# Kernel tuning notes

Hardware: AMD Instinct MI355X
Metric: run time of the kernel (lower is better)

## Reference

```python
import jax, jax.numpy as jnp
import numpy as np

N_BOXES = 1_000_000
EPS = 1e-6


def box2corners(box):
    """(..., 5) [x,y,w,h,angle] -> (..., 4, 2) corners (mmcv box2corners)."""
    x, y, w, h, a = (box[..., i] for i in range(5))
    dx = jnp.asarray([0.5, -0.5, -0.5, 0.5], box.dtype) * w[..., None]  # (...,4)
    dy = jnp.asarray([0.5, 0.5, -0.5, -0.5], box.dtype) * h[..., None]
    cos, sin = jnp.cos(a)[..., None], jnp.sin(a)[..., None]
    cx = dx * cos - dy * sin + x[..., None]
    cy = dx * sin + dy * cos + y[..., None]
    return jnp.stack([cx, cy], axis=-1)


def box_intersection(c1, c2):
    """All 4x4 edge-pair segment intersections. c1,c2: (N,4,2).
    Returns pts (N,4,4,2), mask (N,4,4)."""
    roll = jnp.array([1, 2, 3, 0])
    line1 = jnp.concatenate([c1, c1[:, roll, :]], axis=-1)  # (N,4,4): x1,y1,x2,y2
    line2 = jnp.concatenate([c2, c2[:, roll, :]], axis=-1)
    l1 = line1[:, :, None, :]  # (N,4,1,4)
    l2 = line2[:, None, :, :]  # (N,1,4,4)
    x1, y1, x2, y2 = l1[..., 0], l1[..., 1], l1[..., 2], l1[..., 3]
    x3, y3, x4, y4 = l2[..., 0], l2[..., 1], l2[..., 2], l2[..., 3]
    num = (y4 - y3) * (x2 - x1) - (x4 - x3) * (y2 - y1)
    den_t = (x4 - x3) * (y1 - y3) - (y4 - y3) * (x1 - x3)
    safe = jnp.where(num == 0.0, 1.0, num)
    t = jnp.where(num == 0.0, -1.0, den_t / safe)
    mask_t = (t > 0) & (t < 1)
    den_u = (x2 - x1) * (y1 - y3) - (y2 - y1) * (x1 - x3)
    u = jnp.where(num == 0.0, -1.0, -den_u / safe)
    mask_u = (u > 0) & (u < 1)
    mask = mask_t & mask_u
    t2 = den_t / (num + 1e-8)
    pts = jnp.stack([x1 + t2 * (x2 - x1), y1 + t2 * (y2 - y1)], axis=-1)
    pts = pts * mask[..., None].astype(pts.dtype)
    return pts, mask


def box1_in_box2(c1, c2):
    """Which corners of c1 lie inside box c2. (N,4,2)x(N,4,2)->(N,4) bool."""
    a = c2[:, 0:1, :]
    b = c2[:, 1:2, :]
    d = c2[:, 3:4, :]
    ab, ad, am = b - a, d - a, c1 - a
    pab = jnp.sum(ab * am, -1) / jnp.sum(ab * ab, -1)
    pad_ = jnp.sum(ad * am, -1) / jnp.sum(ad * ad, -1)
    e = 1e-6
    return (pab > -e) & (pab < 1 + e) & (pad_ > -e) & (pad_ < 1 + e)


def intersection_area(c1, c2):
    """Differentiable rotated-box intersection area via convex polygon clipping."""
    inter_pts, inter_mask = box_intersection(c1, c2)
    m1 = box1_in_box2(c1, c2)
    m2 = box1_in_box2(c2, c1)
    n = c1.shape[0]
    verts = jnp.concatenate([c1, c2, inter_pts.reshape(n, 16, 2)], axis=1)  # (N,24,2)
    mask = jnp.concatenate([m1, m2, inter_mask.reshape(n, 16)], axis=1)     # (N,24)
    k = jnp.sum(mask, axis=-1)  # num valid vertices per box
    mf = mask.astype(verts.dtype)
    mean = jnp.sum(verts * mf[..., None], axis=1, keepdims=True) / \
        jnp.maximum(k, 1).astype(verts.dtype)[:, None, None]
    vn = verts - mean
    # sort valid vertices counterclockwise by angle around centroid; invalid last
    ang = jnp.where(mask, jnp.arctan2(vn[..., 1], vn[..., 0]), 1e9)
    order = jnp.argsort(ang, axis=-1)
    vs = jnp.take_along_axis(verts, order[..., None], axis=1)  # (N,24,2)
    idx = jnp.arange(24)
    nxt = jnp.where(idx[None, :] + 1 < k[:, None], idx[None, :] + 1, 0)
    v_next = jnp.take_along_axis(vs, nxt[..., None], axis=1)
    cross = vs[..., 0] * v_next[..., 1] - vs[..., 1] * v_next[..., 0]
    valid = idx[None, :] < k[:, None]
    return jnp.abs(jnp.sum(jnp.where(valid, cross, 0.0), axis=-1)) * 0.5


def fpdiou_loss(pred, target):
    c1 = box2corners(pred)
    c2 = box2corners(target)
    inter = intersection_area(c1, c2)
    area1 = pred[:, 2] * pred[:, 3]
    area2 = target[:, 2] * target[:, 3]
    iou = inter / (area1 + area2 - inter)
    iou = jnp.maximum(iou, EPS)
    # corner-distance term (detached in original via .detach().cpu().numpy())
    p = jax.lax.stop_gradient(c1)
    g = jax.lax.stop_gradient(c2)
    ps = jnp.take_along_axis(p, jnp.argsort(p[..., 0], axis=-1)[..., None], axis=1)
    gs = jnp.take_along_axis(g, jnp.argsort(g[..., 0], axis=-1)[..., None], axis=1)
    d = 2.0 * (gs[:, 0, 0] - ps[:, 0, 0]) ** 2 \
        + (ps[:, 1, 0] - gs[:, 1, 0]) ** 2 + (ps[:, 1, 1] - gs[:, 1, 1]) ** 2 \
        + (ps[:, 2, 0] - gs[:, 2, 0]) ** 2 + (ps[:, 2, 1] - gs[:, 2, 1]) ** 2 \
        + (ps[:, 3, 0] - gs[:, 3, 0]) ** 2 + (ps[:, 3, 1] - gs[:, 3, 1]) ** 2
    res = d / (4.0 * 1024.0 ** 2)
    loss = 1.0 - iou + res  # mode='linear'
    return jnp.mean(loss)   # reduction='mean', loss_weight=1.0


def setup_inputs() -> dict:
    key = jax.random.key(0)
    k1, k2, k3, k4 = jax.random.split(key, 4)
    xy = jax.random.uniform(k1, (N_BOXES, 2), minval=0.0, maxval=1024.0)
    wh = jax.random.uniform(k2, (N_BOXES, 2), minval=8.0, maxval=96.0)
    ang = jax.random.uniform(k3, (N_BOXES, 1), minval=-np.pi / 2, maxval=np.pi / 2)
    pred = jnp.concatenate([xy, wh, ang], axis=-1).astype(jnp.float32)
    scale = jnp.asarray([4.0, 4.0, 3.0, 3.0, 0.1], jnp.float32)
    target = pred + jax.random.normal(k4, (N_BOXES, 5), jnp.float32) * scale
    target = target.at[:, 2:4].set(jnp.maximum(target[:, 2:4], 4.0))
    return {"pred": pred, "target": target}


def reference(pred, target):
    return fpdiou_loss(pred, target)
```

## Files before the change

kernel.cpp:

```cpp
#include <hip/hip_runtime.h>

#define BS 64
#define NVMAX 16

__device__ __forceinline__ void sort4_by_x(const float* x, const float* y,
                                           float* sx, float* sy) {
    int rk[4];
#pragma unroll
    for (int a = 0; a < 4; a++) {
        int r = 0;
#pragma unroll
        for (int b = 0; b < 4; b++) {
            r += (x[b] < x[a]) || (x[b] == x[a] && b < a);
        }
        rk[a] = r;
    }
#pragma unroll
    for (int r = 0; r < 4; r++) {
        float vx = 0.f, vy = 0.f;
#pragma unroll
        for (int a = 0; a < 4; a++) {
            if (rk[a] == r) { vx = x[a]; vy = y[a]; }
        }
        sx[r] = vx; sy[r] = vy;
    }
}

__device__ __forceinline__ float pseudo_angle(float dx, float dy) {
    float s = fabsf(dx) + fabsf(dy);
    float r = (s == 0.f) ? 0.f : (1.f - dx / s);
    return copysignf(r, dy);
}

__global__ __launch_bounds__(BS, 2)
void fpdiou_kernel(const float* __restrict__ pred, const float* __restrict__ tgt,
                   float* __restrict__ partial, int n)
{
    __shared__ float s_vx[NVMAX * BS];
    __shared__ float s_vy[NVMAX * BS];
    __shared__ float s_p [NVMAX * BS];

    const int tid = threadIdx.x;
    const int i = blockIdx.x * BS + tid;
    float loss = 0.f;

    if (i < n) {
        const float* pp = pred + (size_t)i * 5;
        const float* gg = tgt  + (size_t)i * 5;
        const float pw = pp[2], ph = pp[3];
        const float gw = gg[2], gh = gg[3];

        float c1x[4], c1y[4], c2x[4], c2y[4];
        {
            const float DX[4] = {0.5f, -0.5f, -0.5f, 0.5f};
            const float DY[4] = {0.5f,  0.5f, -0.5f, -0.5f};
            float s, c;
            sincosf(pp[4], &s, &c);
            float x = pp[0], y = pp[1];
#pragma unroll
            for (int q = 0; q < 4; q++) {
                float dx = DX[q] * pw, dy = DY[q] * ph;
                c1x[q] = dx * c - dy * s + x;
                c1y[q] = dx * s + dy * c + y;
            }
            sincosf(gg[4], &s, &c);
            x = gg[0]; y = gg[1];
#pragma unroll
            for (int q = 0; q < 4; q++) {
                float dx = DX[q] * gw, dy = DY[q] * gh;
                c2x[q] = dx * c - dy * s + x;
                c2y[q] = dx * s + dy * c + y;
            }
        }

        int k = 0;
        float sx = 0.f, sy = 0.f;
        {
            const float ax = c2x[0], ay = c2y[0];
            const float abx = c2x[1] - ax, aby = c2y[1] - ay;
            const float adx = c2x[3] - ax, ady = c2y[3] - ay;
            const float dab = abx * abx + aby * aby;
            const float dad = adx * adx + ady * ady;
#pragma unroll
            for (int q = 0; q < 4; q++) {
                float amx = c1x[q] - ax, amy = c1y[q] - ay;
                float pab = (abx * amx + aby * amy) / dab;
                float pd  = (adx * amx + ady * amy) / dad;
                const float e = 1e-6f;
                if (pab > -e && pab < 1.f + e && pd > -e && pd < 1.f + e) {
                    s_vx[k * BS + tid] = c1x[q];
                    s_vy[k * BS + tid] = c1y[q];
                    sx += c1x[q]; sy += c1y[q];
                    k++;
                }
            }
        }
        {
            const float ax = c1x[0], ay = c1y[0];
            const float abx = c1x[1] - ax, aby = c1y[1] - ay;
            const float adx = c1x[3] - ax, ady = c1y[3] - ay;
            const float dab = abx * abx + aby * aby;
            const float dad = adx * adx + ady * ady;
#pragma unroll
            for (int q = 0; q < 4; q++) {
                float amx = c2x[q] - ax, amy = c2y[q] - ay;
                float pab = (abx * amx + aby * amy) / dab;
                float pd  = (adx * amx + ady * amy) / dad;
                const float e = 1e-6f;
                if (pab > -e && pab < 1.f + e && pd > -e && pd < 1.f + e) {
                    s_vx[k * BS + tid] = c2x[q];
                    s_vy[k * BS + tid] = c2y[q];
                    sx += c2x[q]; sy += c2y[q];
                    k++;
                }
            }
        }
#pragma unroll
        for (int a = 0; a < 4; a++) {
            const float x1 = c1x[a], y1 = c1y[a];
            const float ex = c1x[(a + 1) & 3] - x1, ey = c1y[(a + 1) & 3] - y1;
#pragma unroll
            for (int b = 0; b < 4; b++) {
                const float x3 = c2x[b], y3 = c2y[b];
                const float fx = c2x[(b + 1) & 3] - x3, fy = c2y[(b + 1) & 3] - y3;
                const float num = fy * ex - fx * ey;
                const float dx13 = x1 - x3, dy13 = y1 - y3;
                const float den_t = fx * dy13 - fy * dx13;
                const float den_u = ex * dy13 - ey * dx13;
                const float t = den_t / num;
                const float u = -den_u / num;
                if (t > 0.f && t < 1.f && u > 0.f && u < 1.f && k < NVMAX) {
                    const float t2 = den_t / (num + 1e-8f);
                    const float ix = x1 + t2 * ex, iy = y1 + t2 * ey;
                    s_vx[k * BS + tid] = ix;
                    s_vy[k * BS + tid] = iy;
                    sx += ix; sy += iy;
                    k++;
                }
            }
        }

        float area = 0.f;
        if (k > 0) {
            const float mx = sx / (float)k;
            const float my = sy / (float)k;
            for (int v = 0; v < k; v++) {
                s_p[v * BS + tid] = pseudo_angle(s_vx[v * BS + tid] - mx,
                                                 s_vy[v * BS + tid] - my);
            }
            int mj = 0;
            float mp = s_p[tid];
            for (int j = 1; j < k; j++) {
                float pj = s_p[j * BS + tid];
                if (pj < mp) { mp = pj; mj = j; }
            }
            float cr = 0.f;
            for (int v = 0; v < k; v++) {
                const float pv = s_p[v * BS + tid];
                float bp = 3.4e38f;
                int bj = -1;
                for (int j = 0; j < k; j++) {
                    float pj = s_p[j * BS + tid];
                    bool gt = (pj > pv) || ((pj == pv) && (j > v));
                    if (gt && pj < bp) { bp = pj; bj = j; }
                }
                const int sj = (bj >= 0) ? bj : mj;
                cr += s_vx[v * BS + tid] * s_vy[sj * BS + tid]
                    - s_vy[v * BS + tid] * s_vx[sj * BS + tid];
            }
            area = fabsf(cr) * 0.5f;
        }

        const float a1 = pw * ph, a2 = gw * gh;
        float iou = area / (a1 + a2 - area);
        iou = fmaxf(iou, 1e-6f);

        float psx[4], psy[4], gsx[4], gsy[4];
        sort4_by_x(c1x, c1y, psx, psy);
        sort4_by_x(c2x, c2y, gsx, gsy);
        const float d0 = gsx[0] - psx[0];
        float d = 2.f * d0 * d0;
#pragma unroll
        for (int q = 1; q < 4; q++) {
            float dxq = psx[q] - gsx[q];
            float dyq = psy[q] - gsy[q];
            d += dxq * dxq + dyq * dyq;
        }
        const float res = d * (1.f / 4194304.f);

        loss = 1.f - iou + res;
    }

#pragma unroll
    for (int off = 32; off > 0; off >>= 1)
        loss += __shfl_down(loss, off, 64);
    if (tid == 0) partial[blockIdx.x] = loss;
}

__global__ __launch_bounds__(1024)
void fpdiou_reduce_kernel(const float* __restrict__ partial, int nblk,
                          float* __restrict__ out, float inv_n)
{
    __shared__ float red[16];
    float s = 0.f;
    for (int i = threadIdx.x; i < nblk; i += blockDim.x)
        s += partial[i];
#pragma unroll
    for (int off = 32; off > 0; off >>= 1)
        s += __shfl_down(s, off, 64);
    if ((threadIdx.x & 63) == 0) red[threadIdx.x >> 6] = s;
    __syncthreads();
    if (threadIdx.x == 0) {
        float t = 0.f;
#pragma unroll
        for (int w = 0; w < 16; w++) t += red[w];
        out[0] = t * inv_n;
    }
}

extern "C" void kernel_launch(void* const* d_in, const int* in_sizes, int n_in,
                              void* d_out, int out_size, void* d_ws, size_t ws_size,
                              hipStream_t stream)
{
    const float* pred = (const float*)d_in[0];
    const float* tgt  = (const float*)d_in[1];
    float* out = (float*)d_out;
    const int n = in_sizes[0] / 5;
    const int nblk = (n + BS - 1) / BS;
    float* partial = (float*)d_ws;

    fpdiou_kernel<<<nblk, BS, 0, stream>>>(pred, tgt, partial, n);
    fpdiou_reduce_kernel<<<1, 1024, 0, stream>>>(partial, nblk, out, 1.f / (float)n);
}
```

Measured before the change: 152.7 us.

## Replace shared-memory polygon sort with register sorting network and atomic reduction

The vertex buffer moves from shared memory to per-thread registers with a validity bitmask. The O(k^2) successor search is replaced by a constexpr Batcher sorting network over 24 fixed slots keyed on pseudo-angle. Divides become hardware reciprocals, the block size goes from 64 to 256, and the second reduce kernel is replaced by block-level atomicAdd after a memset. This removes LDS traffic and divergent loops but raises register pressure, adds fixed sort work for every box, and makes the float atomic summation order nondeterministic.

```diff
diff --git a/kernel.cpp b/kernel.cpp
--- a/kernel.cpp
+++ b/kernel.cpp
@@ -1,7 +1,28 @@
 #include <hip/hip_runtime.h>
 
-#define BS 64
-#define NVMAX 16
+#define BS 256
+#define NS 24
+
+struct CEp { int a, b; };
+struct CEList { CEp p[160]; int n; };
+constexpr CEList make_ce() {
+    CEList L{}; L.n = 0;
+    const int n = NS;
+    int t = 0; while ((1 << t) < n) t++;
+    for (int p = 1 << (t - 1); p > 0; p >>= 1) {
+        int q = 1 << (t - 1), r = 0, d = p;
+        for (;;) {
+            for (int i = 0; i < n - d; i++)
+                if ((i & p) == r) { L.p[L.n].a = i; L.p[L.n].b = i + d; L.n++; }
+            if (q == p) break;
+            d = q - p; q >>= 1; r = p;
+        }
+    }
+    return L;
+}
+constexpr CEList CEL = make_ce();
+
+__device__ __forceinline__ float rcpf(float x) { return __builtin_amdgcn_rcpf(x); }
 
 __device__ __forceinline__ void sort4_by_x(const float* x, const float* y,
                                            float* sx, float* sy) {
@@ -10,36 +31,25 @@
     for (int a = 0; a < 4; a++) {
         int r = 0;
 #pragma unroll
-        for (int b = 0; b < 4; b++) {
+        for (int b = 0; b < 4; b++)
             r += (x[b] < x[a]) || (x[b] == x[a] && b < a);
-        }
         rk[a] = r;
     }
 #pragma unroll
     for (int r = 0; r < 4; r++) {
         float vx = 0.f, vy = 0.f;
 #pragma unroll
-        for (int a = 0; a < 4; a++) {
+        for (int a = 0; a < 4; a++)
             if (rk[a] == r) { vx = x[a]; vy = y[a]; }
-        }
         sx[r] = vx; sy[r] = vy;
     }
-}
-
-__device__ __forceinline__ float pseudo_angle(float dx, float dy) {
-    float s = fabsf(dx) + fabsf(dy);
-    float r = (s == 0.f) ? 0.f : (1.f - dx / s);
-    return copysignf(r, dy);
 }
 
 __global__ __launch_bounds__(BS, 2)
 void fpdiou_kernel(const float* __restrict__ pred, const float* __restrict__ tgt,
-                   float* __restrict__ partial, int n)
+                   float* __restrict__ out, int n, float inv_n)
 {
-    __shared__ float s_vx[NVMAX * BS];
-    __shared__ float s_vy[NVMAX * BS];
-    __shared__ float s_p [NVMAX * BS];
-
+    __shared__ float s_red[BS / 64];
     const int tid = threadIdx.x;
     const int i = blockIdx.x * BS + tid;
     float loss = 0.f;
@@ -47,72 +57,79 @@
     if (i < n) {
         const float* pp = pred + (size_t)i * 5;
         const float* gg = tgt  + (size_t)i * 5;
-        const float pw = pp[2], ph = pp[3];
-        const float gw = gg[2], gh = gg[3];
-
+        const float p0 = pp[0], p1 = pp[1], pw = pp[2], ph = pp[3], pa = pp[4];
+        const float g0 = gg[0], g1 = gg[1], gw = gg[2], gh = gg[3], ga = gg[4];
+
+        float s1, co1, s2, co2;
+        sincosf(pa, &s1, &co1);
+        sincosf(ga, &s2, &co2);
+
+        const float DX[4] = {0.5f, -0.5f, -0.5f, 0.5f};
+        const float DY[4] = {0.5f,  0.5f, -0.5f, -0.5f};
         float c1x[4], c1y[4], c2x[4], c2y[4];
+#pragma unroll
+        for (int q = 0; q < 4; q++) {
+            float dx = DX[q] * pw, dy = DY[q] * ph;
+            c1x[q] = dx * co1 - dy * s1 + p0;
+            c1y[q] = dx * s1 + dy * co1 + p1;
+            dx = DX[q] * gw; dy = DY[q] * gh;
+            c2x[q] = dx * co2 - dy * s2 + g0;
+            c2y[q] = dx * s2 + dy * co2 + g1;
+        }
+
+        float res;
         {
-            const float DX[4] = {0.5f, -0.5f, -0.5f, 0.5f};
-            const float DY[4] = {0.5f,  0.5f, -0.5f, -0.5f};
-            float s, c;
-            sincosf(pp[4], &s, &c);
-            float x = pp[0], y = pp[1];
-#pragma unroll
-            for (int q = 0; q < 4; q++) {
-                float dx = DX[q] * pw, dy = DY[q] * ph;
-                c1x[q] = dx * c - dy * s + x;
-                c1y[q] = dx * s + dy * c + y;
-            }
-            sincosf(gg[4], &s, &c);
-            x = gg[0]; y = gg[1];
-#pragma unroll
-            for (int q = 0; q < 4; q++) {
-                float dx = DX[q] * gw, dy = DY[q] * gh;
-                c2x[q] = dx * c - dy * s + x;
-                c2y[q] = dx * s + dy * c + y;
-            }
-        }
-
+            float psx[4], psy[4], gsx[4], gsy[4];
+            sort4_by_x(c1x, c1y, psx, psy);
+            sort4_by_x(c2x, c2y, gsx, gsy);
+            const float d0 = gsx[0] - psx[0];
+            float d = 2.f * d0 * d0;
+#pragma unroll
+            for (int q = 1; q < 4; q++) {
+                const float dxq = psx[q] - gsx[q];
+                const float dyq = psy[q] - gsy[q];
+                d += dxq * dxq + dyq * dyq;
+            }
+            res = d * (1.f / 4194304.f);
+        }
+
+        float wx[NS], wy[NS];
+        unsigned vm = 0;
+        float sx = 0.f, sy = 0.f;
         int k = 0;
-        float sx = 0.f, sy = 0.f;
+
         {
             const float ax = c2x[0], ay = c2y[0];
             const float abx = c2x[1] - ax, aby = c2y[1] - ay;
             const float adx = c2x[3] - ax, ady = c2y[3] - ay;
-            const float dab = abx * abx + aby * aby;
-            const float dad = adx * adx + ady * ady;
+            const float idab = rcpf(abx * abx + aby * aby);
+            const float idad = rcpf(adx * adx + ady * ady);
 #pragma unroll
             for (int q = 0; q < 4; q++) {
-                float amx = c1x[q] - ax, amy = c1y[q] - ay;
-                float pab = (abx * amx + aby * amy) / dab;
-                float pd  = (adx * amx + ady * amy) / dad;
+                const float amx = c1x[q] - ax, amy = c1y[q] - ay;
+                const float pab = (abx * amx + aby * amy) * idab;
+                const float pd  = (adx * amx + ady * amy) * idad;
                 const float e = 1e-6f;
-                if (pab > -e && pab < 1.f + e && pd > -e && pd < 1.f + e) {
-                    s_vx[k * BS + tid] = c1x[q];
-                    s_vy[k * BS + tid] = c1y[q];
-                    sx += c1x[q]; sy += c1y[q];
-                    k++;
-                }
+                const bool m = (pab > -e) & (pab < 1.f + e) & (pd > -e) & (pd < 1.f + e);
+                wx[q] = c1x[q]; wy[q] = c1y[q];
+                if (m) { vm |= 1u << q; sx += c1x[q]; sy += c1y[q]; k++; }
             }
         }
         {
             const float ax = c1x[0], ay = c1y[0];
             const float abx = c1x[1] - ax, aby = c1y[1] - ay;
             const float adx = c1x[3] - ax, ady = c1y[3] - ay;
-            const float dab = abx * abx + aby * aby;
-            const float dad = adx * adx + ady * ady;
+            const float idab = rcpf(abx * abx + aby * aby);
+            const float idad = rcpf(adx * adx + ady * ady);
 #pragma unroll
             for (int q = 0; q < 4; q++) {
-                float amx = c2x[q] - ax, amy = c2y[q] - ay;
-                float pab = (abx * amx + aby * amy) / dab;
-                float pd  = (adx * amx + ady * amy) / dad;
+                const float amx = c2x[q] - ax, amy = c2y[q] - ay;
+                const float pab = (abx * amx + aby * amy) * idab;
+                const float pd  = (adx * amx + ady * amy) * idad;
                 const float e = 1e-6f;
-                if (pab > -e && pab < 1.f + e && pd > -e && pd < 1.f + e) {
-                    s_vx[k * BS + tid] = c2x[q];
-                    s_vy[k * BS + tid] = c2y[q];
-                    sx += c2x[q]; sy += c2y[q];
-                    k++;
-                }
+                const bool m = (pab > -e) & (pab < 1.f + e) & (pd > -e) & (pd < 1.f + e);
+                wx[4 + q] = c2x[q]; wy[4 + q] = c2y[q];
+                if (m) { vm |= 1u << (4 + q); sx += c2x[q]; sy += c2y[q]; k++; }
             }
         }
 #pragma unroll
@@ -127,94 +144,78 @@
                 const float dx13 = x1 - x3, dy13 = y1 - y3;
                 const float den_t = fx * dy13 - fy * dx13;
                 const float den_u = ex * dy13 - ey * dx13;
-                const float t = den_t / num;
-                const float u = -den_u / num;
-                if (t > 0.f && t < 1.f && u > 0.f && u < 1.f && k < NVMAX) {
-                    const float t2 = den_t / (num + 1e-8f);
-                    const float ix = x1 + t2 * ex, iy = y1 + t2 * ey;
-                    s_vx[k * BS + tid] = ix;
-                    s_vy[k * BS + tid] = iy;
-                    sx += ix; sy += iy;
-                    k++;
-                }
-            }
-        }
-
-        float area = 0.f;
-        if (k > 0) {
-            const float mx = sx / (float)k;
-            const float my = sy / (float)k;
-            for (int v = 0; v < k; v++) {
-                s_p[v * BS + tid] = pseudo_angle(s_vx[v * BS + tid] - mx,
-                                                 s_vy[v * BS + tid] - my);
-            }
-            int mj = 0;
-            float mp = s_p[tid];
-            for (int j = 1; j < k; j++) {
-                float pj = s_p[j * BS + tid];
-                if (pj < mp) { mp = pj; mj = j; }
-            }
-            float cr = 0.f;
-            for (int v = 0; v < k; v++) {
-                const float pv = s_p[v * BS + tid];
-                float bp = 3.4e38f;
-                int bj = -1;
-                for (int j = 0; j < k; j++) {
-                    float pj = s_p[j * BS + tid];
-                    bool gt = (pj > pv) || ((pj == pv) && (j > v));
-                    if (gt && pj < bp) { bp = pj; bj = j; }
-                }
-                const int sj = (bj >= 0) ? bj : mj;
-                cr += s_vx[v * BS + tid] * s_vy[sj * BS + tid]
-                    - s_vy[v * BS + tid] * s_vx[sj * BS + tid];
-            }
-            area = fabsf(cr) * 0.5f;
-        }
+                const float rn = rcpf(num);
+                const float t = den_t * rn;
+                const float u = -den_u * rn;
+                const bool m = (t > 0.f) & (t < 1.f) & (u > 0.f) & (u < 1.f);
+                const float t2 = den_t * rcpf(num + 1e-8f);
+                const float ix = x1 + t2 * ex, iy = y1 + t2 * ey;
+                const int s = 8 + a * 4 + b;
+                wx[s] = m ? ix : 0.f;
+                wy[s] = m ? iy : 0.f;
+                if (m) { vm |= 1u << s; sx += ix; sy += iy; k++; }
+            }
+        }
+
+        const float ik = 1.f / (float)(k > 0 ? k : 1);
+        const float mx = sx * ik, my = sy * ik;
+        unsigned key[NS];
+#pragma unroll
+        for (int s = 0; s < NS; s++) {
+            const float dx = wx[s] - mx, dy = wy[s] - my;
+            const float sa = fabsf(dx) + fabsf(dy);
+            const float r = (sa == 0.f) ? 0.f : (1.f - dx * rcpf(sa));
+            float ang = copysignf(r, dy) + 0.0f;
+            const bool m = (vm >> s) & 1u;
+            ang = m ? ang : 1e9f;
+            unsigned bbits = __float_as_uint(ang);
+            bbits ^= (unsigned)((int)bbits >> 31) | 0x80000000u;
+            key[s] = bbits;
+        }
+
+#pragma unroll
+        for (int c = 0; c < CEL.n; c++) {
+            const int A = CEL.p[c].a, B = CEL.p[c].b;
+            const bool sw = key[B] < key[A];
+            const unsigned ka = sw ? key[B] : key[A];
+            const unsigned kb = sw ? key[A] : key[B];
+            key[A] = ka; key[B] = kb;
+            const float xa = sw ? wx[B] : wx[A];
+            const float xb = sw ? wx[A] : wx[B];
+            wx[A] = xa; wx[B] = xb;
+            const float ya = sw ? wy[B] : wy[A];
+            const float yb = sw ? wy[A] : wy[B];
+            wy[A] = ya; wy[B] = yb;
+        }
+
+        float cr = 0.f;
+#pragma unroll
+        for (int j = 0; j < NS; j++) {
+            const int jn = (j + 1 < NS) ? j + 1 : 0;
+            const bool nw = (j + 1 < k);
+            const float nx = nw ? wx[jn] : wx[0];
+            const float ny = nw ? wy[jn] : wy[0];
+            const float crj = wx[j] * ny - wy[j] * nx;
+            cr += (j < k) ? crj : 0.f;
+        }
+        const float area = fabsf(cr) * 0.5f;
 
         const float a1 = pw * ph, a2 = gw * gh;
         float iou = area / (a1 + a2 - area);
         iou = fmaxf(iou, 1e-6f);
-
-        float psx[4], psy[4], gsx[4], gsy[4];
-        sort4_by_x(c1x, c1y, psx, psy);
-        sort4_by_x(c2x, c2y, gsx, gsy);
-        const float d0 = gsx[0] - psx[0];
-        float d = 2.f * d0 * d0;
-#pragma unroll
-        for (int q = 1; q < 4; q++) {
-            float dxq = psx[q] - gsx[q];
-            float dyq = psy[q] - gsy[q];
-            d += dxq * dxq + dyq * dyq;
-        }
-        const float res = d * (1.f / 4194304.f);
-
         loss = 1.f - iou + res;
     }
 
 #pragma unroll
     for (int off = 32; off > 0; off >>= 1)
         loss += __shfl_down(loss, off, 64);
-    if (tid == 0) partial[blockIdx.x] = loss;
-}
-
-__global__ __launch_bounds__(1024)
-void fpdiou_reduce_kernel(const float* __restrict__ partial, int nblk,
-                          float* __restrict__ out, float inv_n)
-{
-    __shared__ float red[16];
-    float s = 0.f;
-    for (int i = threadIdx.x; i < nblk; i += blockDim.x)
-        s += partial[i];
-#pragma unroll
-    for (int off = 32; off > 0; off >>= 1)
-        s += __shfl_down(s, off, 64);
-    if ((threadIdx.x & 63) == 0) red[threadIdx.x >> 6] = s;
+    if ((tid & 63) == 0) s_red[tid >> 6] = loss;
     __syncthreads();
-    if (threadIdx.x == 0) {
+    if (tid == 0) {
         float t = 0.f;
 #pragma unroll
-        for (int w = 0; w < 16; w++) t += red[w];
-        out[0] = t * inv_n;
+        for (int w = 0; w < BS / 64; w++) t += s_red[w];
+        atomicAdd(out, t * inv_n);
     }
 }
 
@@ -227,8 +228,7 @@
     float* out = (float*)d_out;
     const int n = in_sizes[0] / 5;
     const int nblk = (n + BS - 1) / BS;
-    float* partial = (float*)d_ws;
-
-    fpdiou_kernel<<<nblk, BS, 0, stream>>>(pred, tgt, partial, n);
-    fpdiou_reduce_kernel<<<1, 1024, 0, stream>>>(partial, nblk, out, 1.f / (float)n);
-}
+
+    hipMemsetAsync(out, 0, sizeof(float), stream);
+    fpdiou_kernel<<<nblk, BS, 0, stream>>>(pred, tgt, out, n, 1.f / (float)n);
+}
```

After: 457.1 us. 199% more time.
